# Kernel optimization log

Measured on AMD Instinct MI355X. Metric: run time of the kernel, lower is better.

Reference implementation:

```python
import jax, jax.numpy as jnp
import numpy as np

L, B, S, D, F, H = 4, 2, 1024, 1024, 4096, 16
EPS = 1e-5


def setup_inputs() -> dict:
    key = jax.random.key(0)
    ks = jax.random.split(key, 15)
    w = lambda k, shape, s=0.02: (jax.random.normal(k, shape, jnp.float32) * s)
    inp = {
        "x": jax.random.normal(ks[0], (B, S, D), jnp.float32),
        # stacked per-layer params (scanned over leading L axis)
        "ln1_w": jnp.ones((L, D), jnp.float32),
        "ln1_b": jnp.zeros((L, D), jnp.float32),
        "Wq": w(ks[1], (L, D, D)),
        "Wk": w(ks[2], (L, D, D)),
        "Wv": w(ks[3], (L, D, D)),
        "Wo": w(ks[4], (L, D, D)),
        "bo": jnp.zeros((L, D), jnp.float32),
        "ln2_w": jnp.ones((L, D), jnp.float32),
        "ln2_b": jnp.zeros((L, D), jnp.float32),
        "W1": w(ks[5], (L, D, F)),
        "b1": jnp.zeros((L, F), jnp.float32),
        "W2": w(ks[6], (L, F, D)),
        "b2": jnp.zeros((L, D), jnp.float32),
    }
    return inp


def _layernorm(y, w, b):
    m = jnp.mean(y, axis=-1, keepdims=True)
    v = jnp.mean(jnp.square(y - m), axis=-1, keepdims=True)
    return (y - m) * jax.lax.rsqrt(v + EPS) * w + b


def _block(x, p):
    ln1w, ln1b, wq, wk, wv, wo, bo, ln2w, ln2b, w1, b1, w2, b2 = p
    b, s, d = x.shape
    dh = d // H
    scale = dh ** -0.5
    # --- attention sub-block (pre-norm, residual) ---
    h = _layernorm(x, ln1w, ln1b)
    q = (h @ wq).reshape(b, s, H, dh).transpose(0, 2, 1, 3)  # bhsd
    k = (h @ wk).reshape(b, s, H, dh).transpose(0, 2, 1, 3)
    v = (h @ wv).reshape(b, s, H, dh).transpose(0, 2, 1, 3)
    attn = jax.nn.softmax(jnp.einsum("bhqd,bhkd->bhqk", q, k) * scale, axis=-1)
    o = jnp.einsum("bhqk,bhkd->bhqd", attn, v).transpose(0, 2, 1, 3).reshape(b, s, d)
    x = x + (o @ wo + bo)
    # --- FFN sub-block (pre-norm, residual) ---
    h = _layernorm(x, ln2w, ln2b)
    x = x + (jax.nn.gelu(h @ w1 + b1, approximate=False) @ w2 + b2)
    return x, None


def reference(x, ln1_w, ln1_b, Wq, Wk, Wv, Wo, bo, ln2_w, ln2_b, W1, b1, W2, b2):
    xs = (ln1_w, ln1_b, Wq, Wk, Wv, Wo, bo, ln2_w, ln2_b, W1, b1, W2, b2)
    out, _ = jax.lax.scan(_block, x, xs)
    return out
```

## Files before the change

### kernel.cpp

```cpp
#include <hip/hip_runtime.h>
#include <hip/hip_bf16.h>

using bf16   = __bf16;
using bf16x2 = __attribute__((ext_vector_type(2))) __bf16;
using bf16x4 = __attribute__((ext_vector_type(4))) __bf16;
using bf16x8 = __attribute__((ext_vector_type(8))) __bf16;
using f32x4  = __attribute__((ext_vector_type(4))) float;

constexpr int LAYERS = 4;
constexpr int BATCH  = 2;
constexpr int SEQ    = 1024;
constexpr int DIM    = 1024;
constexpr int FF     = 4096;
constexpr int HEADS  = 16;
constexpr int TOK    = BATCH * SEQ;
constexpr int QKVN   = 3 * DIM;
constexpr float EPS  = 1e-5f;

__device__ __forceinline__ void gload_lds16(const void* g, void* l) {
    __builtin_amdgcn_global_load_lds(
        (const __attribute__((address_space(1))) void*)g,
        (__attribute__((address_space(3))) void*)l, 16, 0, 0);
}

__global__ __launch_bounds__(256) void ln_kernel(
    const float* __restrict__ x, const float* __restrict__ g,
    const float* __restrict__ bt, bf16* __restrict__ out)
{
    __shared__ float red[8];
    const int row = blockIdx.x, t = threadIdx.x;
    const float4 v = ((const float4*)(x + (size_t)row * DIM))[t];

    float s = v.x + v.y + v.z + v.w;
    #pragma unroll
    for (int o = 32; o; o >>= 1) s += __shfl_down(s, o, 64);
    if ((t & 63) == 0) red[t >> 6] = s;
    __syncthreads();
    const float mean = (red[0] + red[1] + red[2] + red[3]) * (1.0f / DIM);

    const float dx = v.x - mean, dy = v.y - mean, dz = v.z - mean, dw = v.w - mean;
    float q = dx * dx + dy * dy + dz * dz + dw * dw;
    #pragma unroll
    for (int o = 32; o; o >>= 1) q += __shfl_down(q, o, 64);
    if ((t & 63) == 0) red[4 + (t >> 6)] = q;
    __syncthreads();
    const float var = (red[4] + red[5] + red[6] + red[7]) * (1.0f / DIM);
    const float rstd = rsqrtf(var + EPS);

    const float4 gg = ((const float4*)g)[t];
    const float4 bb = ((const float4*)bt)[t];
    bf16x4 o4;
    o4[0] = (bf16)(dx * rstd * gg.x + bb.x);
    o4[1] = (bf16)(dy * rstd * gg.y + bb.y);
    o4[2] = (bf16)(dz * rstd * gg.z + bb.z);
    o4[3] = (bf16)(dw * rstd * gg.w + bb.w);
    *(bf16x4*)(out + (size_t)row * DIM + t * 4) = o4;
}

template<bool DO_LN>
__global__ __launch_bounds__(256) void lncomb_kernel(
    float* __restrict__ x, const bf16* __restrict__ p,
    const float* __restrict__ bias, const float* __restrict__ g,
    const float* __restrict__ bt, bf16* __restrict__ out)
{
    __shared__ float red[8];
    const int row = blockIdx.x, t = threadIdx.x;
    float4 v = ((const float4*)(x + (size_t)row * DIM))[t];
    const float4 bv = ((const float4*)bias)[t];
    float a0 = bv.x, a1 = bv.y, a2 = bv.z, a3 = bv.w;
    #pragma unroll
    for (int ks = 0; ks < 4; ++ks) {
        const bf16x4 pp = *(const bf16x4*)(p + (size_t)(ks * TOK + row) * DIM + t * 4);
        a0 += (float)pp[0]; a1 += (float)pp[1];
        a2 += (float)pp[2]; a3 += (float)pp[3];
    }
    v.x += a0; v.y += a1; v.z += a2; v.w += a3;
    ((float4*)(x + (size_t)row * DIM))[t] = v;
    if (!DO_LN) return;

    float s = v.x + v.y + v.z + v.w;
    #pragma unroll
    for (int o = 32; o; o >>= 1) s += __shfl_down(s, o, 64);
    if ((t & 63) == 0) red[t >> 6] = s;
    __syncthreads();
    const float mean = (red[0] + red[1] + red[2] + red[3]) * (1.0f / DIM);

    const float dx = v.x - mean, dy = v.y - mean, dz = v.z - mean, dw = v.w - mean;
    float q = dx * dx + dy * dy + dz * dz + dw * dw;
    #pragma unroll
    for (int o = 32; o; o >>= 1) q += __shfl_down(q, o, 64);
    if ((t & 63) == 0) red[4 + (t >> 6)] = q;
    __syncthreads();
    const float var = (red[4] + red[5] + red[6] + red[7]) * (1.0f / DIM);
    const float rstd = rsqrtf(var + EPS);

    const float4 gg = ((const float4*)g)[t];
    const float4 bb = ((const float4*)bt)[t];
    bf16x4 o4;
    o4[0] = (bf16)(dx * rstd * gg.x + bb.x);
    o4[1] = (bf16)(dy * rstd * gg.y + bb.y);
    o4[2] = (bf16)(dz * rstd * gg.z + bb.z);
    o4[3] = (bf16)(dw * rstd * gg.w + bb.w);
    *(bf16x4*)(out + (size_t)row * DIM + t * 4) = o4;
}

__global__ __launch_bounds__(256) void wtrans_all_kernel(
    const float* __restrict__ Wq, const float* __restrict__ Wk,
    const float* __restrict__ Wv, const float* __restrict__ Wo,
    const float* __restrict__ W1, const float* __restrict__ W2,
    bf16* __restrict__ wqkvt, bf16* __restrict__ wot,
    bf16* __restrict__ w1t, bf16* __restrict__ w2t)
{
    __shared__ float tile[64][65];
    const int bid = blockIdx.x;
    const float* W; bf16* Wt; int N, K, rowoff, bx, by;
    if (bid < 768) {
        const int seg = bid >> 8, r = bid & 255;
        W = (seg == 0) ? Wq : (seg == 1) ? Wk : Wv;
        Wt = wqkvt; N = DIM; K = DIM; rowoff = seg * DIM;
        bx = r & 15; by = r >> 4;
    } else if (bid < 1024) {
        const int r = bid - 768;
        W = Wo; Wt = wot; N = DIM; K = DIM; rowoff = 0;
        bx = r & 15; by = r >> 4;
    } else if (bid < 2048) {
        const int r = bid - 1024;
        W = W1; Wt = w1t; N = FF; K = DIM; rowoff = 0;
        bx = r & 63; by = r >> 6;
    } else {
        const int r = bid - 2048;
        W = W2; Wt = w2t; N = DIM; K = FF; rowoff = 0;
        bx = r & 15; by = r >> 4;
    }
    const int bn = bx * 64, bk = by * 64;
    {
        const int r16 = threadIdx.x >> 4, c4 = (threadIdx.x & 15) * 4;
        #pragma unroll
        for (int i = 0; i < 4; ++i) {
            const int kr = r16 + i * 16;
            const float4 v = *(const float4*)(W + (size_t)(bk + kr) * N + bn + c4);
            tile[kr][c4 + 0] = v.x; tile[kr][c4 + 1] = v.y;
            tile[kr][c4 + 2] = v.z; tile[kr][c4 + 3] = v.w;
        }
    }
    __syncthreads();
    {
        const int n = threadIdx.x >> 2, ch = threadIdx.x & 3;
        #pragma unroll
        for (int i = 0; i < 2; ++i) {
            const int k0 = (ch + i * 4) * 8;
            bf16x8 o;
            #pragma unroll
            for (int j = 0; j < 8; ++j) o[j] = (bf16)tile[k0 + j][n];
            *(bf16x8*)(Wt + (size_t)(rowoff + bn + n) * K + bk + k0) = o;
        }
    }
}

template<int EPI, int SK>
__global__ __launch_bounds__(256) void gemm128_kernel(
    const bf16* __restrict__ A, const bf16* __restrict__ Bt,
    const float* __restrict__ bias, void* __restrict__ outv,
    int M, int N, int Kfull)
{
    __shared__ bf16 As[2][128 * 64];
    __shared__ bf16 Bs[2][128 * 64];

    const int t    = threadIdx.x;
    const int lane = t & 63;
    const int w    = t >> 6;
    const int wm   = (w >> 1) * 64;
    const int wn   = (w & 1) * 64;
    const int kg   = lane >> 4, lr = lane & 15;
    const int key  = lr & 7;

    const int nwg = gridDim.x;
    const int bid = (blockIdx.x & 7) * (nwg >> 3) + (blockIdx.x >> 3);
    const int nbn = N / 128, nbm = M / 128;
    const int ks  = (SK > 1) ? bid / (nbm * nbn) : 0;
    const int r   = (SK > 1) ? bid % (nbm * nbn) : bid;
    const int bm  = ((SK > 1) ? (r / nbn) : (r % nbm)) * 128;
    const int bn  = ((SK > 1) ? (r % nbn) : (r / nbm)) * 128;

    const int Ksl = Kfull / SK;
    const int kof = ks * Ksl;

    f32x4 acc[4][4] = {};

    auto stage = [&](int buf, int k0) {
        #pragma unroll
        for (int it = 0; it < 4; ++it) {
            const int ci = it * 256 + t, row = ci >> 3, c = ci & 7;
            gload_lds16(A + (size_t)(bm + row) * Kfull + kof + k0 + ((c ^ (row & 7)) << 3),
                        &As[buf][ci * 8]);
        }
        #pragma unroll
        for (int it = 0; it < 4; ++it) {
            const int ci = it * 256 + t, row = ci >> 3, c = ci & 7;
            gload_lds16(Bt + (size_t)(bn + row) * Kfull + kof + k0 + ((c ^ (row & 7)) << 3),
                        &Bs[buf][ci * 8]);
        }
    };

    stage(0, 0);
    __syncthreads();

    int cur = 0;
    for (int k0 = 0; k0 < Ksl; k0 += 64) {
        if (k0 + 64 < Ksl) stage(cur ^ 1, k0 + 64);

        #pragma unroll
        for (int kk = 0; kk < 2; ++kk) {
            bf16x8 af[4], bfr[4];
            #pragma unroll
            for (int m = 0; m < 4; ++m) {
                const int row = wm + m * 16 + lr;
                af[m] = *(const bf16x8*)(&As[cur][row * 64 + (((kk * 4 + kg) ^ key) << 3)]);
            }
            #pragma unroll
            for (int n = 0; n < 4; ++n) {
                const int row = wn + n * 16 + lr;
                bfr[n] = *(const bf16x8*)(&Bs[cur][row * 64 + (((kk * 4 + kg) ^ key) << 3)]);
            }
            #pragma unroll
            for (int m = 0; m < 4; ++m)
                #pragma unroll
                for (int n = 0; n < 4; ++n)
                    acc[m][n] = __builtin_amdgcn_mfma_f32_16x16x32_bf16(af[m], bfr[n], acc[m][n], 0, 0, 0);
        }

        __syncthreads();
        cur ^= 1;
    }

    #pragma unroll
    for (int m = 0; m < 4; ++m) {
        const int row = bm + wm + m * 16 + kg * 4;
        #pragma unroll
        for (int n = 0; n < 4; ++n) {
            const int col = bn + wn + n * 16 + lr;
            #pragma unroll
            for (int j = 0; j < 4; ++j) {
                const float vv = acc[m][n][j];
                const size_t idx = (size_t)(row + j) * N + col;
                if (EPI == 0) {
                    ((bf16*)outv)[idx] = (bf16)vv;
                } else if (EPI == 1) {
                    const float z = vv + bias[col];
                    const float gl = 0.5f * z * (1.0f + erff(z * 0.70710678118654752f));
                    ((bf16*)outv)[idx] = (bf16)gl;
                } else {
                    ((bf16*)outv)[(size_t)ks * M * N + idx] = (bf16)vv;
                }
            }
        }
    }
}

template<int EPI, int SK>
__global__ __launch_bounds__(256) void gemm64_kernel(
    const bf16* __restrict__ A, const bf16* __restrict__ Bt,
    const float* __restrict__ bias, void* __restrict__ outv,
    int M, int N, int Kfull)
{
    constexpr int MR = 2;
    __shared__ bf16 As[2][128 * 32];
    __shared__ bf16 Bs[2][64 * 32];

    const int t    = threadIdx.x;
    const int lane = t & 63;
    const int w    = t >> 6;
    const int wm   = w * 32;
    const int kg   = lane >> 4, lr = lane & 15;
    const int key  = (lr >> 1) & 3;

    const int nwg = gridDim.x;
    const int bid = (blockIdx.x & 7) * (nwg >> 3) + (blockIdx.x >> 3);
    const int nbn = N / 64, nbm = M / 128;
    const int ks  = (SK > 1) ? bid / (nbm * nbn) : 0;
    const int r   = (SK > 1) ? bid % (nbm * nbn) : bid;
    const int bm  = ((SK > 1) ? (r / nbn) : (r % nbm)) * 128;
    const int bn  = ((SK > 1) ? (r % nbn) : (r / nbm)) * 64;

    const int Ksl = Kfull / SK;
    const int kof = ks * Ksl;

    f32x4 acc[MR][4] = {};

    auto stage = [&](int buf, int k0) {
        #pragma unroll
        for (int it = 0; it < 2; ++it) {
            const int ci = it * 256 + t, row = ci >> 2, c = ci & 3;
            gload_lds16(A + (size_t)(bm + row) * Kfull + kof + k0 + ((c ^ ((row >> 1) & 3)) << 3),
                        &As[buf][ci * 8]);
        }
        {
            const int ci = t, row = ci >> 2, c = ci & 3;
            gload_lds16(Bt + (size_t)(bn + row) * Kfull + kof + k0 + ((c ^ ((row >> 1) & 3)) << 3),
                        &Bs[buf][ci * 8]);
        }
    };

    stage(0, 0);
    __syncthreads();

    int cur = 0;
    for (int k0 = 0; k0 < Ksl; k0 += 32) {
        if (k0 + 32 < Ksl) stage(cur ^ 1, k0 + 32);

        bf16x8 af[MR], bfr[4];
        #pragma unroll
        for (int m = 0; m < MR; ++m) {
            const int row = wm + m * 16 + lr;
            af[m] = *(const bf16x8*)(&As[cur][row * 32 + ((kg ^ key) << 3)]);
        }
        #pragma unroll
        for (int n = 0; n < 4; ++n) {
            const int row = n * 16 + lr;
            bfr[n] = *(const bf16x8*)(&Bs[cur][row * 32 + ((kg ^ key) << 3)]);
        }
        #pragma unroll
        for (int m = 0; m < MR; ++m)
            #pragma unroll
            for (int n = 0; n < 4; ++n)
                acc[m][n] = __builtin_amdgcn_mfma_f32_16x16x32_bf16(af[m], bfr[n], acc[m][n], 0, 0, 0);

        __syncthreads();
        cur ^= 1;
    }

    #pragma unroll
    for (int m = 0; m < MR; ++m) {
        const int row = bm + wm + m * 16 + kg * 4;
        #pragma unroll
        for (int n = 0; n < 4; ++n) {
            const int col = bn + n * 16 + lr;
            #pragma unroll
            for (int j = 0; j < 4; ++j) {
                const float vv = acc[m][n][j];
                const size_t idx = (size_t)(row + j) * N + col;
                if (EPI == 0) {
                    ((bf16*)outv)[idx] = (bf16)vv;
                } else if (EPI == 1) {
                    const float z = vv + bias[col];
                    const float gl = 0.5f * z * (1.0f + erff(z * 0.70710678118654752f));
                    ((bf16*)outv)[idx] = (bf16)gl;
                } else {
                    ((bf16*)outv)[(size_t)ks * M * N + idx] = (bf16)vv;
                }
            }
        }
    }
}

__global__ __launch_bounds__(256) void attn_kernel(
    const bf16* __restrict__ qkv, bf16* __restrict__ od)
{
    __shared__ bf16 Ks[2][64 * 64];
    __shared__ bf16 Vt[2][64][64];
    __shared__ bf16 Ps[4][16][72];

    const int nwg = gridDim.x;
    const int bid = (blockIdx.x & 7) * (nwg >> 3) + (blockIdx.x >> 3);
    const int q0  = (bid & 15) * 64;
    const int bh  = bid >> 4;
    const int b   = bh >> 4, h = bh & 15;
    const int t   = threadIdx.x, w = t >> 6, lane = t & 63;
    const int kg  = lane >> 4, lr = lane & 15;

    const bf16* qbase = qkv + (size_t)b * SEQ * QKVN + h * 64;
    const bf16* kbase = qbase + DIM;
    const bf16* vbase = qbase + 2 * DIM;

    bf16x8 qf0, qf1;
    {
        const bf16* qr = qbase + (size_t)(q0 + w * 16 + lr) * QKVN;
        qf0 = *(const bf16x8*)(qr + kg * 8);
        qf1 = *(const bf16x8*)(qr + 32 + kg * 8);
        #pragma unroll
        for (int j = 0; j < 8; ++j) {
            qf0[j] = (bf16)((float)qf0[j] * 0.125f);
            qf1[j] = (bf16)((float)qf1[j] * 0.125f);
        }
    }

    f32x4 o_acc[4] = {};
    float m_run = -1e30f, l_run = 0.f;

    const int rp = t >> 3, cV = t & 7;

    bf16x8 vr0, vr1;
    auto loadV = [&](int kb) {
        vr0 = *(const bf16x8*)(vbase + (size_t)(kb + 2 * rp) * QKVN + cV * 8);
        vr1 = *(const bf16x8*)(vbase + (size_t)(kb + 2 * rp + 1) * QKVN + cV * 8);
    };
    auto stageK = [&](int buf, int kb) {
        #pragma unroll
        for (int i = 0; i < 2; ++i) {
            const int ci = i * 256 + t, row = ci >> 3, c = ci & 7;
            gload_lds16(kbase + (size_t)(kb + row) * QKVN + ((c ^ (row & 7)) << 3),
                        &Ks[buf][ci * 8]);
        }
    };
    auto storeV = [&](int buf) {
        #pragma unroll
        for (int j = 0; j < 8; ++j) {
            bf16x2 p; p[0] = vr0[j]; p[1] = vr1[j];
            const int d  = cV * 8 + j;
            const int dw = (((rp >> 2) ^ (j ^ cV)) << 2) | (rp & 3);
            *(bf16x2*)((char*)&Vt[buf][d][0] + dw * 4) = p;
        }
    };

    loadV(0);
    stageK(0, 0);
    storeV(0);
    __syncthreads();

    int cur = 0;
    for (int kb = 0; kb < SEQ; kb += 64) {
        const bool more = (kb + 64 < SEQ);
        if (more) { loadV(kb + 64); stageK(cur ^ 1, kb + 64); }

        f32x4 s[4] = {};
        __builtin_amdgcn_s_setprio(1);
        #pragma unroll
        for (int n = 0; n < 4; ++n) {
            const int row = n * 16 + lr;
            const bf16x8 kf0 = *(const bf16x8*)&Ks[cur][row * 64 + ((kg ^ (lr & 7)) << 3)];
            const bf16x8 kf1 = *(const bf16x8*)&Ks[cur][row * 64 + (((4 + kg) ^ (lr & 7)) << 3)];
            s[n] = __builtin_amdgcn_mfma_f32_16x16x32_bf16(kf0, qf0, s[n], 0, 0, 0);
            s[n] = __builtin_amdgcn_mfma_f32_16x16x32_bf16(kf1, qf1, s[n], 0, 0, 0);
        }
        __builtin_amdgcn_s_setprio(0);

        float pmax = -1e30f;
        #pragma unroll
        for (int n = 0; n < 4; ++n)
            #pragma unroll
            for (int j = 0; j < 4; ++j) pmax = fmaxf(pmax, s[n][j]);
        pmax = fmaxf(pmax, __shfl_xor(pmax, 16, 64));
        pmax = fmaxf(pmax, __shfl_xor(pmax, 32, 64));

        if (!__all(pmax <= m_run + 8.0f)) {
            const float mn   = fmaxf(m_run, pmax);
            const float corr = __expf(m_run - mn);
            m_run = mn;
            l_run *= corr;
            #pragma unroll
            for (int nd = 0; nd < 4; ++nd)
                #pragma unroll
                for (int j = 0; j < 4; ++j) o_acc[nd][j] *= corr;
        }

        float rs = 0.f;
        #pragma unroll
        for (int n = 0; n < 4; ++n)
            #pragma unroll
            for (int j = 0; j < 4; ++j) {
                const float e = __expf(s[n][j] - m_run);
                s[n][j] = e; rs += e;
            }
        rs += __shfl_xor(rs, 16, 64);
        rs += __shfl_xor(rs, 32, 64);
        l_run += rs;

        #pragma unroll
        for (int n = 0; n < 4; ++n) {
            bf16x4 pw;
            #pragma unroll
            for (int j = 0; j < 4; ++j) pw[j] = (bf16)s[n][j];
            *(bf16x4*)&Ps[w][lr][n * 16 + kg * 4] = pw;
        }

        const bf16x8 pf0 = *(const bf16x8*)&Ps[w][lr][kg * 8];
        const bf16x8 pf1 = *(const bf16x8*)&Ps[w][lr][32 + kg * 8];
        __builtin_amdgcn_s_setprio(1);
        #pragma unroll
        for (int nd = 0; nd < 4; ++nd) {
            const int d   = nd * 16 + lr;
            const int keyv = (d ^ (d >> 3)) & 7;
            const bf16x8 vf0 = *(const bf16x8*)((const char*)&Vt[cur][d][0] + ((kg ^ keyv) << 4));
            const bf16x8 vf1 = *(const bf16x8*)((const char*)&Vt[cur][d][0] + (((4 + kg) ^ keyv) << 4));
            o_acc[nd] = __builtin_amdgcn_mfma_f32_16x16x32_bf16(vf0, pf0, o_acc[nd], 0, 0, 0);
            o_acc[nd] = __builtin_amdgcn_mfma_f32_16x16x32_bf16(vf1, pf1, o_acc[nd], 0, 0, 0);
        }
        __builtin_amdgcn_s_setprio(0);

        if (more) storeV(cur ^ 1);
        __syncthreads();
        cur ^= 1;
    }

    const float inv = 1.0f / l_run;
    bf16* ob = od + (size_t)(b * SEQ + q0 + w * 16 + lr) * DIM + h * 64;
    #pragma unroll
    for (int nd = 0; nd < 4; ++nd) {
        bf16x4 o4;
        #pragma unroll
        for (int j = 0; j < 4; ++j) o4[j] = (bf16)(o_acc[nd][j] * inv);
        *(bf16x4*)(ob + nd * 16 + kg * 4) = o4;
    }
}

extern "C" void kernel_launch(void* const* d_in, const int* in_sizes, int n_in,
                              void* d_out, int out_size, void* d_ws, size_t ws_size,
                              hipStream_t stream)
{
    const float* x    = (const float*)d_in[0];
    const float* ln1w = (const float*)d_in[1];
    const float* ln1b = (const float*)d_in[2];
    const float* Wq   = (const float*)d_in[3];
    const float* Wk   = (const float*)d_in[4];
    const float* Wv   = (const float*)d_in[5];
    const float* Wo   = (const float*)d_in[6];
    const float* bo   = (const float*)d_in[7];
    const float* ln2w = (const float*)d_in[8];
    const float* ln2b = (const float*)d_in[9];
    const float* W1   = (const float*)d_in[10];
    const float* b1   = (const float*)d_in[11];
    const float* W2   = (const float*)d_in[12];
    const float* b2   = (const float*)d_in[13];

    char* ws = (char*)d_ws;
    float* xbuf  = (float*)(ws);
    bf16*  hbuf  = (bf16*)(ws + (8ull  << 20));
    bf16*  qkvb  = (bf16*)(ws + (12ull << 20));
    bf16*  obuf  = (bf16*)(ws + (24ull << 20));
    bf16*  gbuf  = (bf16*)(ws + (28ull << 20));
    bf16*  wqkvt = (bf16*)(ws + (44ull << 20));
    bf16*  wot   = (bf16*)(ws + (50ull << 20));
    bf16*  w1t   = (bf16*)(ws + (52ull << 20));
    bf16*  w2t   = (bf16*)(ws + (60ull << 20));
    bf16*  pbuf  = (bf16*)(ws + (68ull << 20));

    hipMemcpyAsync(xbuf, x, (size_t)TOK * DIM * sizeof(float),
                   hipMemcpyDeviceToDevice, stream);

    const size_t DD = (size_t)DIM * DIM, DF = (size_t)DIM * FF;
    for (int l = 0; l < LAYERS; ++l) {
        wtrans_all_kernel<<<3072, 256, 0, stream>>>(
            Wq + l * DD, Wk + l * DD, Wv + l * DD, Wo + l * DD,
            W1 + l * DF, W2 + l * DF, wqkvt, wot, w1t, w2t);

        if (l == 0)
            ln_kernel<<<TOK, 256, 0, stream>>>(xbuf, ln1w, ln1b, hbuf);

        gemm128_kernel<0, 1><<<16 * 24, 256, 0, stream>>>(
            hbuf, wqkvt, nullptr, qkvb, TOK, QKVN, DIM);

        attn_kernel<<<512, 256, 0, stream>>>(qkvb, obuf);

        gemm64_kernel<3, 4><<<16 * 16 * 4, 256, 0, stream>>>(
            obuf, wot, nullptr, pbuf, TOK, DIM, DIM);

        lncomb_kernel<true><<<TOK, 256, 0, stream>>>(
            xbuf, pbuf, bo + l * DIM, ln2w + l * DIM, ln2b + l * DIM, hbuf);

        gemm128_kernel<1, 1><<<16 * 32, 256, 0, stream>>>(
            hbuf, w1t, b1 + l * FF, gbuf, TOK, FF, DIM);

        gemm128_kernel<3, 4><<<16 * 8 * 4, 256, 0, stream>>>(
            gbuf, w2t, nullptr, pbuf, TOK, DIM, FF);

        if (l + 1 < LAYERS)
            lncomb_kernel<true><<<TOK, 256, 0, stream>>>(
                xbuf, pbuf, b2 + l * DIM, ln1w + (l + 1) * DIM, ln1b + (l + 1) * DIM, hbuf);
        else
            lncomb_kernel<false><<<TOK, 256, 0, stream>>>(
                xbuf, pbuf, b2 + l * DIM, nullptr, nullptr, nullptr);
    }

    hipMemcpyAsync(d_out, xbuf, (size_t)TOK * DIM * sizeof(float),
                   hipMemcpyDeviceToDevice, stream);
}
```

Measured before the change: 586.1 us.

## Split attention over two key halves and batch weight transposes into one launch

Attention now splits each query tile's key range into two halves, doubling the grid from 512 to 1024 workgroups. Each half writes partial outputs plus running max and sum, and a new combine kernel merges them with log-sum-exp weights. Separately, the four per-layer weight-transpose launches become one 12288-block launch that writes all layers' transposed weights into distinct workspace regions. This is meant to improve occupancy in attention and cut launch overhead, at the cost of an extra kernel, extra partial-output traffic, and a larger workspace.

```diff
diff --git a/kernel.cpp b/kernel.cpp
--- a/kernel.cpp
+++ b/kernel.cpp
@@ -108,28 +108,35 @@
     const float* __restrict__ Wq, const float* __restrict__ Wk,
     const float* __restrict__ Wv, const float* __restrict__ Wo,
     const float* __restrict__ W1, const float* __restrict__ W2,
-    bf16* __restrict__ wqkvt, bf16* __restrict__ wot,
-    bf16* __restrict__ w1t, bf16* __restrict__ w2t)
+    char* __restrict__ wsW)
 {
     __shared__ float tile[64][65];
-    const int bid = blockIdx.x;
+    const int l   = blockIdx.x / 3072;
+    const int bid = blockIdx.x - l * 3072;
+    const size_t DD = (size_t)DIM * DIM, DF = (size_t)DIM * FF;
+    char* base = wsW + (size_t)l * (24ull << 20);
+    bf16* wqkvt = (bf16*)(base);
+    bf16* wot   = (bf16*)(base + (6ull  << 20));
+    bf16* w1t   = (bf16*)(base + (8ull  << 20));
+    bf16* w2t   = (bf16*)(base + (16ull << 20));
+
     const float* W; bf16* Wt; int N, K, rowoff, bx, by;
     if (bid < 768) {
         const int seg = bid >> 8, r = bid & 255;
-        W = (seg == 0) ? Wq : (seg == 1) ? Wk : Wv;
+        W = ((seg == 0) ? Wq : (seg == 1) ? Wk : Wv) + l * DD;
         Wt = wqkvt; N = DIM; K = DIM; rowoff = seg * DIM;
         bx = r & 15; by = r >> 4;
     } else if (bid < 1024) {
         const int r = bid - 768;
-        W = Wo; Wt = wot; N = DIM; K = DIM; rowoff = 0;
+        W = Wo + l * DD; Wt = wot; N = DIM; K = DIM; rowoff = 0;
         bx = r & 15; by = r >> 4;
     } else if (bid < 2048) {
         const int r = bid - 1024;
-        W = W1; Wt = w1t; N = FF; K = DIM; rowoff = 0;
+        W = W1 + l * DF; Wt = w1t; N = FF; K = DIM; rowoff = 0;
         bx = r & 63; by = r >> 6;
     } else {
         const int r = bid - 2048;
-        W = W2; Wt = w2t; N = DIM; K = FF; rowoff = 0;
+        W = W2 + l * DF; Wt = w2t; N = DIM; K = FF; rowoff = 0;
         bx = r & 15; by = r >> 4;
     }
     const int bn = bx * 64, bk = by * 64;
@@ -354,7 +361,8 @@
 }
 
 __global__ __launch_bounds__(256) void attn_kernel(
-    const bf16* __restrict__ qkv, bf16* __restrict__ od)
+    const bf16* __restrict__ qkv, bf16* __restrict__ opart,
+    float2* __restrict__ ml)
 {
     __shared__ bf16 Ks[2][64 * 64];
     __shared__ bf16 Vt[2][64][64];
@@ -363,7 +371,8 @@
     const int nwg = gridDim.x;
     const int bid = (blockIdx.x & 7) * (nwg >> 3) + (blockIdx.x >> 3);
     const int q0  = (bid & 15) * 64;
-    const int bh  = bid >> 4;
+    const int kh  = (bid >> 4) & 1;
+    const int bh  = bid >> 5;
     const int b   = bh >> 4, h = bh & 15;
     const int t   = threadIdx.x, w = t >> 6, lane = t & 63;
     const int kg  = lane >> 4, lr = lane & 15;
@@ -412,14 +421,15 @@
         }
     };
 
-    loadV(0);
-    stageK(0, 0);
+    const int kb0 = kh * 512;
+    loadV(kb0);
+    stageK(0, kb0);
     storeV(0);
     __syncthreads();
 
     int cur = 0;
-    for (int kb = 0; kb < SEQ; kb += 64) {
-        const bool more = (kb + 64 < SEQ);
+    for (int kb = kb0; kb < kb0 + 512; kb += 64) {
+        const bool more = (kb + 64 < kb0 + 512);
         if (more) { loadV(kb + 64); stageK(cur ^ 1, kb + 64); }
 
         f32x4 s[4] = {};
@@ -492,8 +502,10 @@
         cur ^= 1;
     }
 
+    const int q = q0 + w * 16 + lr;
     const float inv = 1.0f / l_run;
-    bf16* ob = od + (size_t)(b * SEQ + q0 + w * 16 + lr) * DIM + h * 64;
+    bf16* ob = opart + (size_t)kh * TOK * DIM
+                     + (size_t)(b * SEQ + q) * DIM + h * 64;
     #pragma unroll
     for (int nd = 0; nd < 4; ++nd) {
         bf16x4 o4;
@@ -501,6 +513,35 @@
         for (int j = 0; j < 4; ++j) o4[j] = (bf16)(o_acc[nd][j] * inv);
         *(bf16x4*)(ob + nd * 16 + kg * 4) = o4;
     }
+    if (kg == 0)
+        ml[(size_t)kh * (BATCH * HEADS * SEQ) + ((b * HEADS + h) << 10) + q]
+            = make_float2(m_run, l_run);
+}
+
+__global__ __launch_bounds__(256) void attn_comb_kernel(
+    const bf16* __restrict__ op, const float2* __restrict__ ml,
+    bf16* __restrict__ od)
+{
+    const int r = blockIdx.x;
+    const int t = threadIdx.x;
+    const int h = t >> 4;
+    const int b = r >> 10, q = r & 1023;
+    const int mi = ((b * HEADS + h) << 10) + q;
+    const float2 p1 = ml[mi];
+    const float2 p2 = ml[BATCH * HEADS * SEQ + mi];
+    const float m  = fmaxf(p1.x, p2.x);
+    const float w1 = p1.y * __expf(p1.x - m);
+    const float w2 = p2.y * __expf(p2.x - m);
+    const float inv = 1.0f / (w1 + w2);
+    const float a = w1 * inv, c = w2 * inv;
+    const size_t idx = (size_t)r * DIM + t * 4;
+    const bf16x4 o1 = *(const bf16x4*)(op + idx);
+    const bf16x4 o2 = *(const bf16x4*)(op + (size_t)TOK * DIM + idx);
+    bf16x4 o;
+    #pragma unroll
+    for (int j = 0; j < 4; ++j)
+        o[j] = (bf16)(a * (float)o1[j] + c * (float)o2[j]);
+    *(bf16x4*)(od + idx) = o;
 }
 
 extern "C" void kernel_launch(void* const* d_in, const int* in_sizes, int n_in,
@@ -523,25 +564,27 @@
     const float* b2   = (const float*)d_in[13];
 
     char* ws = (char*)d_ws;
-    float* xbuf  = (float*)(ws);
-    bf16*  hbuf  = (bf16*)(ws + (8ull  << 20));
-    bf16*  qkvb  = (bf16*)(ws + (12ull << 20));
-    bf16*  obuf  = (bf16*)(ws + (24ull << 20));
-    bf16*  gbuf  = (bf16*)(ws + (28ull << 20));
-    bf16*  wqkvt = (bf16*)(ws + (44ull << 20));
-    bf16*  wot   = (bf16*)(ws + (50ull << 20));
-    bf16*  w1t   = (bf16*)(ws + (52ull << 20));
-    bf16*  w2t   = (bf16*)(ws + (60ull << 20));
-    bf16*  pbuf  = (bf16*)(ws + (68ull << 20));
+    float*  xbuf  = (float*)(ws);
+    bf16*   hbuf  = (bf16*)(ws + (8ull  << 20));
+    bf16*   qkvb  = (bf16*)(ws + (12ull << 20));
+    bf16*   obuf  = (bf16*)(ws + (24ull << 20));
+    bf16*   gbuf  = (bf16*)(ws + (28ull << 20));
+    bf16*   pbuf  = (bf16*)(ws + (44ull << 20));
+    bf16*   opart = (bf16*)(ws + (60ull << 20));
+    float2* mlbuf = (float2*)(ws + (68ull << 20));
+    char*   wsW   = ws + (72ull << 20);
 
     hipMemcpyAsync(xbuf, x, (size_t)TOK * DIM * sizeof(float),
                    hipMemcpyDeviceToDevice, stream);
 
-    const size_t DD = (size_t)DIM * DIM, DF = (size_t)DIM * FF;
+    wtrans_all_kernel<<<12288, 256, 0, stream>>>(Wq, Wk, Wv, Wo, W1, W2, wsW);
+
     for (int l = 0; l < LAYERS; ++l) {
-        wtrans_all_kernel<<<3072, 256, 0, stream>>>(
-            Wq + l * DD, Wk + l * DD, Wv + l * DD, Wo + l * DD,
-            W1 + l * DF, W2 + l * DF, wqkvt, wot, w1t, w2t);
+        char* base = wsW + (size_t)l * (24ull << 20);
+        bf16* wqkvt = (bf16*)(base);
+        bf16* wot   = (bf16*)(base + (6ull  << 20));
+        bf16* w1t   = (bf16*)(base + (8ull  << 20));
+        bf16* w2t   = (bf16*)(base + (16ull << 20));
 
         if (l == 0)
             ln_kernel<<<TOK, 256, 0, stream>>>(xbuf, ln1w, ln1b, hbuf);
@@ -549,7 +592,8 @@
         gemm128_kernel<0, 1><<<16 * 24, 256, 0, stream>>>(
             hbuf, wqkvt, nullptr, qkvb, TOK, QKVN, DIM);
 
-        attn_kernel<<<512, 256, 0, stream>>>(qkvb, obuf);
+        attn_kernel<<<1024, 256, 0, stream>>>(qkvb, opart, mlbuf);
+        attn_comb_kernel<<<TOK, 256, 0, stream>>>(opart, mlbuf, obuf);
 
         gemm64_kernel<3, 4><<<16 * 16 * 4, 256, 0, stream>>>(
             obuf, wot, nullptr, pbuf, TOK, DIM, DIM);
```

Result: slower. 618.9 us (+5.6%).
